# Optimization experiments

Hardware: AMD Instinct MI355X
Metric: run time of the kernel (lower is better)

The kernel has to match this reference:

```python
import jax, jax.numpy as jnp
import numpy as np

SQRT_HALF = np.float32(np.sqrt(0.5))
H_AX, W_AX = 2, 3


def _refl_idx(idx, r):
    # symmetric extension with edge repetition (np.pad mode='symmetric'),
    # identical to dtcwt's reflect(idx, -0.5, r-0.5). Static numpy computation.
    idx = np.mod(idx, 2 * r)
    return np.where(idx < r, idx, 2 * r - 1 - idx)


def _filt(X, h, axis):
    # Non-decimating 1-D filtering (dtcwt colfilter/rowfilter): symmetric pad by
    # len(h)//2, true convolution, 'valid' -> output same length as input.
    X = jnp.moveaxis(X, axis, -1)
    m = h.shape[0]
    m2 = m // 2
    L = X.shape[-1]
    Xp = jnp.pad(X, [(0, 0)] * (X.ndim - 1) + [(m2, m2)], mode='symmetric')
    out = sum(h[m - 1 - j] * Xp[..., j:j + L] for j in range(m))  # flip -> convolution
    return jnp.moveaxis(out, -1, axis)


def _dfilt(X, ha, hb, highpass, axis):
    # Decimate-by-2 dual-tree filtering (dtcwt coldfilt/rowdfilt).
    # ha filters one polyphase stream, hb the other; outputs are interleaved.
    X = jnp.moveaxis(X, axis, -1)
    r = X.shape[-1]
    assert r % 4 == 0, 'filtered dim must be a multiple of 4'
    m = ha.shape[0]
    m2 = m // 2
    xe = _refl_idx(np.arange(-m, r + m), r)        # symmetric-extended indices
    t = np.arange(5, r + 2 * m - 2, 4)             # 0-based MATLAB t = 6:4:r+2m-2
    hao, hae = ha[0::2], ha[1::2]
    hbo, hbe = hb[0::2], hb[1::2]

    def cv(rows, f):
        # 'valid' true convolution along gathered (stride-4) sample sequence
        A = X[..., rows]
        Lout = rows.shape[0] - m2 + 1              # == r // 4
        return sum(f[m2 - 1 - j] * A[..., j:j + Lout] for j in range(m2))

    ya = cv(xe[t - 1], hao) + cv(xe[t - 3], hae)
    yb = cv(xe[t], hbo) + cv(xe[t - 2], hbe)
    first, second = (yb, ya) if highpass else (ya, yb)
    Y = jnp.stack([first, second], axis=-1).reshape(X.shape[:-1] + (r // 2,))
    return jnp.moveaxis(Y, -1, axis)


def _q2c(y):
    # quads -> two complex subimages: p = (a+jb)/sqrt2, q = (d-jc)/sqrt2; z = p -/+ q
    a = y[..., 0::2, 0::2]
    b = y[..., 0::2, 1::2]
    c = y[..., 1::2, 0::2]
    d = y[..., 1::2, 1::2]
    z1 = ((a - d) * SQRT_HALF, (b + c) * SQRT_HALF)
    z2 = ((a + d) * SQRT_HALF, (b - c) * SQRT_HALF)
    return z1, z2


def _bands_to_yh(lh, hl, hh):
    # orientation order 15,45,75,105,135,165 degrees; output [N,C,6,H',W',2]
    (r15, i15), (r165, i165) = _q2c(lh)
    (r45, i45), (r135, i135) = _q2c(hh)
    (r75, i75), (r105, i105) = _q2c(hl)
    reals = jnp.stack([r15, r45, r75, r105, r135, r165], axis=2)
    imags = jnp.stack([i15, i45, i75, i105, i135, i165], axis=2)
    return jnp.stack([reals, imags], axis=-1)


def _dtcwt_fwd(x, h0o, h1o, h0a, h0b, h1a, h1b, J=3):
    # Level 1: non-decimating biorthogonal filters
    lo = _filt(x, h0o, W_AX)
    hi = _filt(x, h1o, W_AX)
    ll = _filt(lo, h0o, H_AX)
    yh = [_bands_to_yh(_filt(lo, h1o, H_AX),   # lh
                       _filt(hi, h0o, H_AX),   # hl
                       _filt(hi, h1o, H_AX))]  # hh
    # Levels 2..J: decimating qshift filters
    for _ in range(1, J):
        lo = _dfilt(ll, h0b, h0a, False, W_AX)
        hi = _dfilt(ll, h1b, h1a, True, W_AX)
        ll = _dfilt(lo, h0b, h0a, False, H_AX)
        yh.append(_bands_to_yh(_dfilt(lo, h1b, h1a, True, H_AX),
                               _dfilt(hi, h0b, h0a, False, H_AX),
                               _dfilt(hi, h1b, h1a, True, H_AX)))
    return (ll, *yh)


def setup_inputs() -> dict:
    key = jax.random.key(0)
    ks = jax.random.split(key, 5)
    x = jax.random.normal(ks[0], (4, 16, 512, 512), dtype=jnp.float32)

    def mk(k, n):
        h = jax.random.normal(k, (n,), dtype=jnp.float32)
        return h / jnp.linalg.norm(h)  # unit-norm to keep levels well scaled

    h0o = mk(ks[1], 5)
    h1o = mk(ks[2], 7)
    h0a = mk(ks[3], 10)
    h1a = mk(ks[4], 10)
    h0b = h0a[::-1]  # dual-tree property: tree-b = time-reversed tree-a
    h1b = h1a[::-1]
    return {'x': x, 'h0o': h0o, 'h1o': h1o, 'h0a': h0a, 'h0b': h0b,
            'h1a': h1a, 'h1b': h1b}


def reference(x, h0o, h1o, h0a, h0b, h1a, h1b):
    # Returns (yl, yh_level1, yh_level2, yh_level3)
    return _dtcwt_fwd(x, h0o, h1o, h0a, h0b, h1a, h1b, J=3)
```

## Files before the change

### kernel.cpp

```cpp
#include <hip/hip_runtime.h>

#define S1 512
#define NIMG 64

__device__ __forceinline__ int refl(int a, int L) {
    a = (a < 0) ? (-a - 1) : a;
    a = (a >= L) ? (2 * L - 1 - a) : a;
    return a;
}

__global__ __launch_bounds__(256) void k_level1(
    const float* __restrict__ x,
    const float* __restrict__ h0o_g, const float* __restrict__ h1o_g,
    float* __restrict__ ll1, float* __restrict__ yh0)
{
    __shared__ float xs[70 * 71];
    __shared__ float lo_s[70 * 65];
    __shared__ float hi_s[70 * 65];

    const int t  = threadIdx.x;
    const int c0 = blockIdx.x * 64;
    const int r0 = blockIdx.y * 64;
    const int n  = blockIdx.z;
    const float* __restrict__ xn = x + (size_t)n * (S1 * S1);

    float f0[5], f1[7];
#pragma unroll
    for (int i = 0; i < 5; ++i) f0[i] = h0o_g[i];
#pragma unroll
    for (int i = 0; i < 7; ++i) f1[i] = h1o_g[i];

    for (int l = t; l < 70 * 70; l += 256) {
        int rl = l / 70, cl = l - rl * 70;
        int ar = refl(r0 - 3 + rl, S1);
        int ac = refl(c0 - 3 + cl, S1);
        xs[rl * 71 + cl] = xn[(size_t)ar * S1 + ac];
    }
    __syncthreads();

    for (int l = t; l < 70 * 64; l += 256) {
        int rl = l >> 6, cl = l & 63;
        const float* xr = &xs[rl * 71 + cl];
        float v0 = xr[0], v1 = xr[1], v2 = xr[2], v3 = xr[3],
              v4 = xr[4], v5 = xr[5], v6 = xr[6];
        float lo = f0[0]*v5 + f0[1]*v4 + f0[2]*v3 + f0[3]*v2 + f0[4]*v1;
        float hi = f1[0]*v6 + f1[1]*v5 + f1[2]*v4 + f1[3]*v3 + f1[4]*v2
                 + f1[5]*v1 + f1[6]*v0;
        lo_s[rl * 65 + cl] = lo;
        hi_s[rl * 65 + cl] = hi;
    }
    __syncthreads();

    const float SQH = 0.70710678118654752440f;
    float* __restrict__ yhn = yh0 + (size_t)n * (6 * 256 * 256 * 2);
    float* __restrict__ lln = ll1 + (size_t)n * (S1 * S1);
    for (int q = t; q < 32 * 32; q += 256) {
        int qi = q >> 5, qj = q & 31;
        float llq[2][2], lhq[2][2], hlq[2][2], hhq[2][2];
#pragma unroll
        for (int cc = 0; cc < 2; ++cc) {
            const int col = 2 * qj + cc;
            float L[8];
#pragma unroll
            for (int j = 0; j < 8; ++j) L[j] = lo_s[(2 * qi + j) * 65 + col];
            llq[0][cc] = f0[0]*L[5] + f0[1]*L[4] + f0[2]*L[3] + f0[3]*L[2] + f0[4]*L[1];
            llq[1][cc] = f0[0]*L[6] + f0[1]*L[5] + f0[2]*L[4] + f0[3]*L[3] + f0[4]*L[2];
            lhq[0][cc] = f1[0]*L[6] + f1[1]*L[5] + f1[2]*L[4] + f1[3]*L[3]
                       + f1[4]*L[2] + f1[5]*L[1] + f1[6]*L[0];
            lhq[1][cc] = f1[0]*L[7] + f1[1]*L[6] + f1[2]*L[5] + f1[3]*L[4]
                       + f1[4]*L[3] + f1[5]*L[2] + f1[6]*L[1];
#pragma unroll
            for (int j = 0; j < 8; ++j) L[j] = hi_s[(2 * qi + j) * 65 + col];
            hlq[0][cc] = f0[0]*L[5] + f0[1]*L[4] + f0[2]*L[3] + f0[3]*L[2] + f0[4]*L[1];
            hlq[1][cc] = f0[0]*L[6] + f0[1]*L[5] + f0[2]*L[4] + f0[3]*L[3] + f0[4]*L[2];
            hhq[0][cc] = f1[0]*L[6] + f1[1]*L[5] + f1[2]*L[4] + f1[3]*L[3]
                       + f1[4]*L[2] + f1[5]*L[1] + f1[6]*L[0];
            hhq[1][cc] = f1[0]*L[7] + f1[1]*L[6] + f1[2]*L[5] + f1[3]*L[4]
                       + f1[4]*L[3] + f1[5]*L[2] + f1[6]*L[1];
        }
        const int oy = r0 + 2 * qi, ox = c0 + 2 * qj;
        float2 w;
        w.x = llq[0][0]; w.y = llq[0][1];
        *(float2*)&lln[(size_t)oy * S1 + ox] = w;
        w.x = llq[1][0]; w.y = llq[1][1];
        *(float2*)&lln[(size_t)(oy + 1) * S1 + ox] = w;

        const int i2 = (r0 >> 1) + qi, j2 = (c0 >> 1) + qj;
        const size_t bs = 256 * 256 * 2;
        float* __restrict__ p = yhn + ((size_t)i2 * 256 + j2) * 2;
        w.x = (lhq[0][0] - lhq[1][1]) * SQH; w.y = (lhq[0][1] + lhq[1][0]) * SQH; *(float2*)(p + 0 * bs) = w;
        w.x = (hhq[0][0] - hhq[1][1]) * SQH; w.y = (hhq[0][1] + hhq[1][0]) * SQH; *(float2*)(p + 1 * bs) = w;
        w.x = (hlq[0][0] - hlq[1][1]) * SQH; w.y = (hlq[0][1] + hlq[1][0]) * SQH; *(float2*)(p + 2 * bs) = w;
        w.x = (hlq[0][0] + hlq[1][1]) * SQH; w.y = (hlq[0][1] - hlq[1][0]) * SQH; *(float2*)(p + 3 * bs) = w;
        w.x = (hhq[0][0] + hhq[1][1]) * SQH; w.y = (hhq[0][1] - hhq[1][0]) * SQH; *(float2*)(p + 4 * bs) = w;
        w.x = (lhq[0][0] + lhq[1][1]) * SQH; w.y = (lhq[0][1] - lhq[1][0]) * SQH; *(float2*)(p + 5 * bs) = w;
    }
}

__global__ __launch_bounds__(256) void k_dfilt(
    const float* __restrict__ X, const int r,
    const float* __restrict__ h0a_g, const float* __restrict__ h0b_g,
    const float* __restrict__ h1a_g, const float* __restrict__ h1b_g,
    float* __restrict__ llo, float* __restrict__ yh)
{
    __shared__ float Xs[80 * 84];
    __shared__ float lo_s[80 * 33];
    __shared__ float hi_s[80 * 33];

    const int t  = threadIdx.x;
    const int x0 = blockIdx.x * 32;
    const int y0 = blockIdx.y * 32;
    const int n  = blockIdx.z;
    const float* __restrict__ Xn = X + (size_t)n * r * r;
    const int cb = 2 * x0 - 8, rb = 2 * y0 - 8;

    float fa0[10], fb0[10], fa1[10], fb1[10];
#pragma unroll
    for (int i = 0; i < 10; ++i) {
        fa0[i] = h0a_g[i]; fb0[i] = h0b_g[i];
        fa1[i] = h1a_g[i]; fb1[i] = h1b_g[i];
    }

    for (int l = t; l < 80 * 80; l += 256) {
        int rl = l / 80, cl = l - rl * 80;
        int ar = refl(rb + rl, r);
        int ac = refl(cb + cl, r);
        Xs[rl * 84 + cl] = Xn[(size_t)ar * r + ac];
    }
    __syncthreads();

    {
        const int cl = t & 31;
        const bool ev = (cl & 1) == 0;
        float cL[20], cH[20];
#pragma unroll
        for (int j = 0; j < 20; ++j) { cL[j] = 0.f; cH[j] = 0.f; }
#pragma unroll
        for (int k = 0; k < 10; ++k) {
            cL[18 - 2 * k] = ev ? fb0[k] : 0.f;
            cL[19 - 2 * k] = ev ? cL[19 - 2 * k] : fa0[k];
            cH[19 - 2 * k] = ev ? fa1[k] : cH[19 - 2 * k];
            cH[18 - 2 * k] = ev ? cH[18 - 2 * k] : fb1[k];
        }
        const int base = 2 * cl - (ev ? 0 : 2);
        for (int rl = (t >> 5); rl < 80; rl += 8) {
            const float* Vp = &Xs[rl * 84 + base];
            float V[20];
#pragma unroll
            for (int j = 0; j < 5; ++j) {
                float4 v = *(const float4*)(Vp + 4 * j);
                V[4*j+0] = v.x; V[4*j+1] = v.y; V[4*j+2] = v.z; V[4*j+3] = v.w;
            }
            float lo = 0.f, hi = 0.f;
#pragma unroll
            for (int j = 0; j < 20; ++j) { lo += cL[j] * V[j]; hi += cH[j] * V[j]; }
            lo_s[rl * 33 + cl] = lo;
            hi_s[rl * 33 + cl] = hi;
        }
    }
    __syncthreads();

    {
        const int qi = t >> 4, qj = t & 15;
        float llq[2][2], lhq[2][2], hlq[2][2], hhq[2][2];
#pragma unroll
        for (int cc = 0; cc < 2; ++cc) {
            const int col = 2 * qj + cc;
            float L[20];
#pragma unroll
            for (int j = 0; j < 20; ++j) L[j] = lo_s[(4 * qi + j) * 33 + col];
            float ll_e = 0.f, ll_o = 0.f, lh_e = 0.f, lh_o = 0.f;
#pragma unroll
            for (int k = 0; k < 10; ++k) {
                float le = L[18 - 2 * k], lod = L[19 - 2 * k];
                ll_e += fb0[k] * le;
                ll_o += fa0[k] * lod;
                lh_e += fa1[k] * lod;
                lh_o += fb1[k] * le;
            }
            llq[0][cc] = ll_e; llq[1][cc] = ll_o;
            lhq[0][cc] = lh_e; lhq[1][cc] = lh_o;
#pragma unroll
            for (int j = 0; j < 20; ++j) L[j] = hi_s[(4 * qi + j) * 33 + col];
            float hl_e = 0.f, hl_o = 0.f, hh_e = 0.f, hh_o = 0.f;
#pragma unroll
            for (int k = 0; k < 10; ++k) {
                float he = L[18 - 2 * k], ho = L[19 - 2 * k];
                hl_e += fb0[k] * he;
                hl_o += fa0[k] * ho;
                hh_e += fa1[k] * ho;
                hh_o += fb1[k] * he;
            }
            hlq[0][cc] = hl_e; hlq[1][cc] = hl_o;
            hhq[0][cc] = hh_e; hhq[1][cc] = hh_o;
        }

        const int R = r >> 1, R2 = r >> 2;
        const int oy = y0 + 2 * qi, ox = x0 + 2 * qj;
        float2 w;
        w.x = llq[0][0]; w.y = llq[0][1];
        *(float2*)&llo[((size_t)n * R + oy) * R + ox] = w;
        w.x = llq[1][0]; w.y = llq[1][1];
        *(float2*)&llo[((size_t)n * R + oy + 1) * R + ox] = w;

        const float SQH = 0.70710678118654752440f;
        const int i2 = (y0 >> 1) + qi, j2 = (x0 >> 1) + qj;
        const size_t bs = (size_t)R2 * R2 * 2;
        float* __restrict__ p = yh + (size_t)n * 6 * bs + ((size_t)i2 * R2 + j2) * 2;
        w.x = (lhq[0][0] - lhq[1][1]) * SQH; w.y = (lhq[0][1] + lhq[1][0]) * SQH; *(float2*)(p + 0 * bs) = w;
        w.x = (hhq[0][0] - hhq[1][1]) * SQH; w.y = (hhq[0][1] + hhq[1][0]) * SQH; *(float2*)(p + 1 * bs) = w;
        w.x = (hlq[0][0] - hlq[1][1]) * SQH; w.y = (hlq[0][1] + hlq[1][0]) * SQH; *(float2*)(p + 2 * bs) = w;
        w.x = (hlq[0][0] + hlq[1][1]) * SQH; w.y = (hlq[0][1] - hlq[1][0]) * SQH; *(float2*)(p + 3 * bs) = w;
        w.x = (hhq[0][0] + hhq[1][1]) * SQH; w.y = (hhq[0][1] - hhq[1][0]) * SQH; *(float2*)(p + 4 * bs) = w;
        w.x = (lhq[0][0] + lhq[1][1]) * SQH; w.y = (lhq[0][1] - lhq[1][0]) * SQH; *(float2*)(p + 5 * bs) = w;
    }
}

extern "C" void kernel_launch(void* const* d_in, const int* in_sizes, int n_in,
                              void* d_out, int out_size, void* d_ws, size_t ws_size,
                              hipStream_t stream) {
    const float* x   = (const float*)d_in[0];
    const float* h0o = (const float*)d_in[1];
    const float* h1o = (const float*)d_in[2];
    const float* h0a = (const float*)d_in[3];
    const float* h0b = (const float*)d_in[4];
    const float* h1a = (const float*)d_in[5];
    const float* h1b = (const float*)d_in[6];

    float* out = (float*)d_out;
    float* ll3 = out;
    float* yh0 = out + 1048576;
    float* yh1 = out + 51380224;
    float* yh2 = out + 63963136;

    float* ll1 = (float*)d_ws;
    float* ll2 = ll1 + 16777216;

    k_level1<<<dim3(8, 8, NIMG), 256, 0, stream>>>(x, h0o, h1o, ll1, yh0);
    k_dfilt<<<dim3(8, 8, NIMG), 256, 0, stream>>>(ll1, 512, h0a, h0b, h1a, h1b, ll2, yh1);
    k_dfilt<<<dim3(4, 4, NIMG), 256, 0, stream>>>(ll2, 256, h0a, h0b, h1a, h1b, ll3, yh2);
}
```

Baseline: 428.6 us.

## Vectorize tile loads and LDS accesses, split level-1 tile into row halves

The level-1 kernel now processes its 64x64 tile in two 32-row halves, which shrinks shared memory per block. Interior tiles load input columns with float4 global reads, and the row-filter and quad stages use float4 LDS reads and writes. The decimating kernel also uses a float4 fast path for interior loads, and each thread computes an even/odd output pair from one 20-sample window, stored and re-read as float2 from a padded layout. The aim is fewer memory instructions and better occupancy. The cost is recomputing halo rows in each level-1 half and an extra sync per half.

```diff
diff --git a/kernel.cpp b/kernel.cpp
--- a/kernel.cpp
+++ b/kernel.cpp
@@ -14,15 +14,17 @@
     const float* __restrict__ h0o_g, const float* __restrict__ h1o_g,
     float* __restrict__ ll1, float* __restrict__ yh0)
 {
-    __shared__ float xs[70 * 71];
-    __shared__ float lo_s[70 * 65];
-    __shared__ float hi_s[70 * 65];
+    __shared__ float xs[38 * 72];
+    __shared__ float lo_s[38 * 68];
+    __shared__ float hi_s[38 * 68];
 
     const int t  = threadIdx.x;
     const int c0 = blockIdx.x * 64;
     const int r0 = blockIdx.y * 64;
     const int n  = blockIdx.z;
-    const float* __restrict__ xn = x + (size_t)n * (S1 * S1);
+    const float* __restrict__ xn  = x   + (size_t)n * (S1 * S1);
+    float* __restrict__ lln       = ll1 + (size_t)n * (S1 * S1);
+    float* __restrict__ yhn       = yh0 + (size_t)n * (6 * 256 * 256 * 2);
 
     float f0[5], f1[7];
 #pragma unroll
@@ -30,70 +32,115 @@
 #pragma unroll
     for (int i = 0; i < 7; ++i) f1[i] = h1o_g[i];
 
-    for (int l = t; l < 70 * 70; l += 256) {
-        int rl = l / 70, cl = l - rl * 70;
-        int ar = refl(r0 - 3 + rl, S1);
-        int ac = refl(c0 - 3 + cl, S1);
-        xs[rl * 71 + cl] = xn[(size_t)ar * S1 + ac];
-    }
-    __syncthreads();
-
-    for (int l = t; l < 70 * 64; l += 256) {
-        int rl = l >> 6, cl = l & 63;
-        const float* xr = &xs[rl * 71 + cl];
-        float v0 = xr[0], v1 = xr[1], v2 = xr[2], v3 = xr[3],
-              v4 = xr[4], v5 = xr[5], v6 = xr[6];
-        float lo = f0[0]*v5 + f0[1]*v4 + f0[2]*v3 + f0[3]*v2 + f0[4]*v1;
-        float hi = f1[0]*v6 + f1[1]*v5 + f1[2]*v4 + f1[3]*v3 + f1[4]*v2
-                 + f1[5]*v1 + f1[6]*v0;
-        lo_s[rl * 65 + cl] = lo;
-        hi_s[rl * 65 + cl] = hi;
-    }
-    __syncthreads();
-
+    const bool colfast = (c0 >= 4) && (c0 + 67 < S1);
     const float SQH = 0.70710678118654752440f;
-    float* __restrict__ yhn = yh0 + (size_t)n * (6 * 256 * 256 * 2);
-    float* __restrict__ lln = ll1 + (size_t)n * (S1 * S1);
-    for (int q = t; q < 32 * 32; q += 256) {
-        int qi = q >> 5, qj = q & 31;
-        float llq[2][2], lhq[2][2], hlq[2][2], hhq[2][2];
-#pragma unroll
-        for (int cc = 0; cc < 2; ++cc) {
-            const int col = 2 * qj + cc;
-            float L[8];
-#pragma unroll
-            for (int j = 0; j < 8; ++j) L[j] = lo_s[(2 * qi + j) * 65 + col];
-            llq[0][cc] = f0[0]*L[5] + f0[1]*L[4] + f0[2]*L[3] + f0[3]*L[2] + f0[4]*L[1];
-            llq[1][cc] = f0[0]*L[6] + f0[1]*L[5] + f0[2]*L[4] + f0[3]*L[3] + f0[4]*L[2];
-            lhq[0][cc] = f1[0]*L[6] + f1[1]*L[5] + f1[2]*L[4] + f1[3]*L[3]
-                       + f1[4]*L[2] + f1[5]*L[1] + f1[6]*L[0];
-            lhq[1][cc] = f1[0]*L[7] + f1[1]*L[6] + f1[2]*L[5] + f1[3]*L[4]
-                       + f1[4]*L[3] + f1[5]*L[2] + f1[6]*L[1];
-#pragma unroll
-            for (int j = 0; j < 8; ++j) L[j] = hi_s[(2 * qi + j) * 65 + col];
-            hlq[0][cc] = f0[0]*L[5] + f0[1]*L[4] + f0[2]*L[3] + f0[3]*L[2] + f0[4]*L[1];
-            hlq[1][cc] = f0[0]*L[6] + f0[1]*L[5] + f0[2]*L[4] + f0[3]*L[3] + f0[4]*L[2];
-            hhq[0][cc] = f1[0]*L[6] + f1[1]*L[5] + f1[2]*L[4] + f1[3]*L[3]
-                       + f1[4]*L[2] + f1[5]*L[1] + f1[6]*L[0];
-            hhq[1][cc] = f1[0]*L[7] + f1[1]*L[6] + f1[2]*L[5] + f1[3]*L[4]
-                       + f1[4]*L[3] + f1[5]*L[2] + f1[6]*L[1];
-        }
-        const int oy = r0 + 2 * qi, ox = c0 + 2 * qj;
-        float2 w;
-        w.x = llq[0][0]; w.y = llq[0][1];
-        *(float2*)&lln[(size_t)oy * S1 + ox] = w;
-        w.x = llq[1][0]; w.y = llq[1][1];
-        *(float2*)&lln[(size_t)(oy + 1) * S1 + ox] = w;
-
-        const int i2 = (r0 >> 1) + qi, j2 = (c0 >> 1) + qj;
-        const size_t bs = 256 * 256 * 2;
-        float* __restrict__ p = yhn + ((size_t)i2 * 256 + j2) * 2;
-        w.x = (lhq[0][0] - lhq[1][1]) * SQH; w.y = (lhq[0][1] + lhq[1][0]) * SQH; *(float2*)(p + 0 * bs) = w;
-        w.x = (hhq[0][0] - hhq[1][1]) * SQH; w.y = (hhq[0][1] + hhq[1][0]) * SQH; *(float2*)(p + 1 * bs) = w;
-        w.x = (hlq[0][0] - hlq[1][1]) * SQH; w.y = (hlq[0][1] + hlq[1][0]) * SQH; *(float2*)(p + 2 * bs) = w;
-        w.x = (hlq[0][0] + hlq[1][1]) * SQH; w.y = (hlq[0][1] - hlq[1][0]) * SQH; *(float2*)(p + 3 * bs) = w;
-        w.x = (hhq[0][0] + hhq[1][1]) * SQH; w.y = (hhq[0][1] - hhq[1][0]) * SQH; *(float2*)(p + 4 * bs) = w;
-        w.x = (lhq[0][0] + lhq[1][1]) * SQH; w.y = (lhq[0][1] - lhq[1][0]) * SQH; *(float2*)(p + 5 * bs) = w;
+
+    for (int h = 0; h < 2; ++h) {
+        const int gr0 = r0 + 32 * h - 3;
+
+        if (colfast) {
+            for (int l = t; l < 38 * 18; l += 256) {
+                int rl = l / 18, cf = l - rl * 18;
+                int ar = refl(gr0 + rl, S1);
+                float4 v = *(const float4*)&xn[(size_t)ar * S1 + (c0 - 4) + 4 * cf];
+                *(float4*)&xs[rl * 72 + 4 * cf] = v;
+            }
+        } else {
+            for (int l = t; l < 38 * 72; l += 256) {
+                int rl = l / 72, cl = l - rl * 72;
+                xs[rl * 72 + cl] =
+                    xn[(size_t)refl(gr0 + rl, S1) * S1 + refl(c0 - 4 + cl, S1)];
+            }
+        }
+        __syncthreads();
+
+        for (int l = t; l < 38 * 16; l += 256) {
+            int rl = l >> 4, cg = l & 15;
+            const float* p = &xs[rl * 72 + 4 * cg];
+            float4 va = *(const float4*)p;
+            float4 vb = *(const float4*)(p + 4);
+            float4 vc = *(const float4*)(p + 8);
+            float V[12] = {va.x, va.y, va.z, va.w, vb.x, vb.y, vb.z, vb.w,
+                           vc.x, vc.y, vc.z, vc.w};
+            float lov[4], hiv[4];
+#pragma unroll
+            for (int cc = 0; cc < 4; ++cc) {
+                lov[cc] = f0[0]*V[cc+6] + f0[1]*V[cc+5] + f0[2]*V[cc+4]
+                        + f0[3]*V[cc+3] + f0[4]*V[cc+2];
+                hiv[cc] = f1[0]*V[cc+7] + f1[1]*V[cc+6] + f1[2]*V[cc+5]
+                        + f1[3]*V[cc+4] + f1[4]*V[cc+3] + f1[5]*V[cc+2]
+                        + f1[6]*V[cc+1];
+            }
+            *(float4*)&lo_s[rl * 68 + 4 * cg] = make_float4(lov[0], lov[1], lov[2], lov[3]);
+            *(float4*)&hi_s[rl * 68 + 4 * cg] = make_float4(hiv[0], hiv[1], hiv[2], hiv[3]);
+        }
+        __syncthreads();
+
+        {
+            const int qi = t >> 4, cg = t & 15;
+            float4 Lv[8];
+            float llv[2][4], lhv[2][4], hlv[2][4], hhv[2][4];
+
+#pragma unroll
+            for (int j = 0; j < 8; ++j)
+                Lv[j] = *(const float4*)&lo_s[(2 * qi + j) * 68 + 4 * cg];
+            {
+                const float* L = (const float*)Lv;
+#pragma unroll
+                for (int cc = 0; cc < 4; ++cc) {
+                    float Lc[8];
+#pragma unroll
+                    for (int j = 0; j < 8; ++j) Lc[j] = L[4 * j + cc];
+                    llv[0][cc] = f0[0]*Lc[5] + f0[1]*Lc[4] + f0[2]*Lc[3] + f0[3]*Lc[2] + f0[4]*Lc[1];
+                    llv[1][cc] = f0[0]*Lc[6] + f0[1]*Lc[5] + f0[2]*Lc[4] + f0[3]*Lc[3] + f0[4]*Lc[2];
+                    lhv[0][cc] = f1[0]*Lc[6] + f1[1]*Lc[5] + f1[2]*Lc[4] + f1[3]*Lc[3]
+                               + f1[4]*Lc[2] + f1[5]*Lc[1] + f1[6]*Lc[0];
+                    lhv[1][cc] = f1[0]*Lc[7] + f1[1]*Lc[6] + f1[2]*Lc[5] + f1[3]*Lc[4]
+                               + f1[4]*Lc[3] + f1[5]*Lc[2] + f1[6]*Lc[1];
+                }
+            }
+#pragma unroll
+            for (int j = 0; j < 8; ++j)
+                Lv[j] = *(const float4*)&hi_s[(2 * qi + j) * 68 + 4 * cg];
+            {
+                const float* L = (const float*)Lv;
+#pragma unroll
+                for (int cc = 0; cc < 4; ++cc) {
+                    float Lc[8];
+#pragma unroll
+                    for (int j = 0; j < 8; ++j) Lc[j] = L[4 * j + cc];
+                    hlv[0][cc] = f0[0]*Lc[5] + f0[1]*Lc[4] + f0[2]*Lc[3] + f0[3]*Lc[2] + f0[4]*Lc[1];
+                    hlv[1][cc] = f0[0]*Lc[6] + f0[1]*Lc[5] + f0[2]*Lc[4] + f0[3]*Lc[3] + f0[4]*Lc[2];
+                    hhv[0][cc] = f1[0]*Lc[6] + f1[1]*Lc[5] + f1[2]*Lc[4] + f1[3]*Lc[3]
+                               + f1[4]*Lc[2] + f1[5]*Lc[1] + f1[6]*Lc[0];
+                    hhv[1][cc] = f1[0]*Lc[7] + f1[1]*Lc[6] + f1[2]*Lc[5] + f1[3]*Lc[4]
+                               + f1[4]*Lc[3] + f1[5]*Lc[2] + f1[6]*Lc[1];
+                }
+            }
+
+            const int oy = r0 + 32 * h + 2 * qi, ox = c0 + 4 * cg;
+            *(float4*)&lln[(size_t)oy * S1 + ox] =
+                make_float4(llv[0][0], llv[0][1], llv[0][2], llv[0][3]);
+            *(float4*)&lln[(size_t)(oy + 1) * S1 + ox] =
+                make_float4(llv[1][0], llv[1][1], llv[1][2], llv[1][3]);
+
+            const int i2 = (r0 >> 1) + 16 * h + qi, j2 = (c0 >> 1) + 2 * cg;
+            const size_t bs = 256 * 256 * 2;
+            float* __restrict__ p = yhn + ((size_t)i2 * 256 + j2) * 2;
+#define BAND_Z1(X0, X1) make_float4((X0[0]-X1[1])*SQH, (X0[1]+X1[0])*SQH, \
+                                    (X0[2]-X1[3])*SQH, (X0[3]+X1[2])*SQH)
+#define BAND_Z2(X0, X1) make_float4((X0[0]+X1[1])*SQH, (X0[1]-X1[0])*SQH, \
+                                    (X0[2]+X1[3])*SQH, (X0[3]-X1[2])*SQH)
+            *(float4*)(p + 0 * bs) = BAND_Z1(lhv[0], lhv[1]);
+            *(float4*)(p + 1 * bs) = BAND_Z1(hhv[0], hhv[1]);
+            *(float4*)(p + 2 * bs) = BAND_Z1(hlv[0], hlv[1]);
+            *(float4*)(p + 3 * bs) = BAND_Z2(hlv[0], hlv[1]);
+            *(float4*)(p + 4 * bs) = BAND_Z2(hhv[0], hhv[1]);
+            *(float4*)(p + 5 * bs) = BAND_Z2(lhv[0], lhv[1]);
+#undef BAND_Z1
+#undef BAND_Z2
+        }
+        __syncthreads();
     }
 }
 
@@ -104,8 +151,8 @@
     float* __restrict__ llo, float* __restrict__ yh)
 {
     __shared__ float Xs[80 * 84];
-    __shared__ float lo_s[80 * 33];
-    __shared__ float hi_s[80 * 33];
+    __shared__ float lo_s[80 * 36];
+    __shared__ float hi_s[80 * 36];
 
     const int t  = threadIdx.x;
     const int x0 = blockIdx.x * 32;
@@ -121,92 +168,102 @@
         fa1[i] = h1a_g[i]; fb1[i] = h1b_g[i];
     }
 
-    for (int l = t; l < 80 * 80; l += 256) {
-        int rl = l / 80, cl = l - rl * 80;
-        int ar = refl(rb + rl, r);
-        int ac = refl(cb + cl, r);
-        Xs[rl * 84 + cl] = Xn[(size_t)ar * r + ac];
+    const bool colfast = (cb >= 0) && (cb + 79 < r);
+
+    if (colfast) {
+        for (int l = t; l < 80 * 20; l += 256) {
+            int rl = l / 20, cf = l - rl * 20;
+            int ar = refl(rb + rl, r);
+            float4 v = *(const float4*)&Xn[(size_t)ar * r + cb + 4 * cf];
+            *(float4*)&Xs[rl * 84 + 4 * cf] = v;
+        }
+    } else {
+        for (int l = t; l < 80 * 80; l += 256) {
+            int rl = l / 80, cl = l - rl * 80;
+            Xs[rl * 84 + cl] = Xn[(size_t)refl(rb + rl, r) * r + refl(cb + cl, r)];
+        }
     }
     __syncthreads();
 
+    for (int l = t; l < 80 * 16; l += 256) {
+        int rl = l >> 4, cp = l & 15;
+        const float* p = &Xs[rl * 84 + 4 * cp];
+        float V[20];
+#pragma unroll
+        for (int j = 0; j < 5; ++j) {
+            float4 v = *(const float4*)(p + 4 * j);
+            V[4*j+0] = v.x; V[4*j+1] = v.y; V[4*j+2] = v.z; V[4*j+3] = v.w;
+        }
+        float lo_e = 0.f, lo_o = 0.f, hi_e = 0.f, hi_o = 0.f;
+#pragma unroll
+        for (int k = 0; k < 10; ++k) {
+            float ve = V[18 - 2 * k], vo = V[19 - 2 * k];
+            lo_e += fb0[k] * ve;
+            lo_o += fa0[k] * vo;
+            hi_e += fa1[k] * vo;
+            hi_o += fb1[k] * ve;
+        }
+        *(float2*)&lo_s[rl * 36 + 2 * cp] = make_float2(lo_e, lo_o);
+        *(float2*)&hi_s[rl * 36 + 2 * cp] = make_float2(hi_e, hi_o);
+    }
+    __syncthreads();
+
     {
-        const int cl = t & 31;
-        const bool ev = (cl & 1) == 0;
-        float cL[20], cH[20];
-#pragma unroll
-        for (int j = 0; j < 20; ++j) { cL[j] = 0.f; cH[j] = 0.f; }
-#pragma unroll
-        for (int k = 0; k < 10; ++k) {
-            cL[18 - 2 * k] = ev ? fb0[k] : 0.f;
-            cL[19 - 2 * k] = ev ? cL[19 - 2 * k] : fa0[k];
-            cH[19 - 2 * k] = ev ? fa1[k] : cH[19 - 2 * k];
-            cH[18 - 2 * k] = ev ? cH[18 - 2 * k] : fb1[k];
-        }
-        const int base = 2 * cl - (ev ? 0 : 2);
-        for (int rl = (t >> 5); rl < 80; rl += 8) {
-            const float* Vp = &Xs[rl * 84 + base];
-            float V[20];
-#pragma unroll
-            for (int j = 0; j < 5; ++j) {
-                float4 v = *(const float4*)(Vp + 4 * j);
-                V[4*j+0] = v.x; V[4*j+1] = v.y; V[4*j+2] = v.z; V[4*j+3] = v.w;
-            }
-            float lo = 0.f, hi = 0.f;
-#pragma unroll
-            for (int j = 0; j < 20; ++j) { lo += cL[j] * V[j]; hi += cH[j] * V[j]; }
-            lo_s[rl * 33 + cl] = lo;
-            hi_s[rl * 33 + cl] = hi;
-        }
-    }
-    __syncthreads();
-
-    {
-        const int qi = t >> 4, qj = t & 15;
+        const int qi = t >> 4, cg = t & 15;
+        float2 Lv[20];
         float llq[2][2], lhq[2][2], hlq[2][2], hhq[2][2];
-#pragma unroll
-        for (int cc = 0; cc < 2; ++cc) {
-            const int col = 2 * qj + cc;
-            float L[20];
-#pragma unroll
-            for (int j = 0; j < 20; ++j) L[j] = lo_s[(4 * qi + j) * 33 + col];
-            float ll_e = 0.f, ll_o = 0.f, lh_e = 0.f, lh_o = 0.f;
-#pragma unroll
-            for (int k = 0; k < 10; ++k) {
-                float le = L[18 - 2 * k], lod = L[19 - 2 * k];
-                ll_e += fb0[k] * le;
-                ll_o += fa0[k] * lod;
-                lh_e += fa1[k] * lod;
-                lh_o += fb1[k] * le;
-            }
-            llq[0][cc] = ll_e; llq[1][cc] = ll_o;
-            lhq[0][cc] = lh_e; lhq[1][cc] = lh_o;
-#pragma unroll
-            for (int j = 0; j < 20; ++j) L[j] = hi_s[(4 * qi + j) * 33 + col];
-            float hl_e = 0.f, hl_o = 0.f, hh_e = 0.f, hh_o = 0.f;
-#pragma unroll
-            for (int k = 0; k < 10; ++k) {
-                float he = L[18 - 2 * k], ho = L[19 - 2 * k];
-                hl_e += fb0[k] * he;
-                hl_o += fa0[k] * ho;
-                hh_e += fa1[k] * ho;
-                hh_o += fb1[k] * he;
-            }
-            hlq[0][cc] = hl_e; hlq[1][cc] = hl_o;
-            hhq[0][cc] = hh_e; hhq[1][cc] = hh_o;
+
+#pragma unroll
+        for (int j = 0; j < 20; ++j)
+            Lv[j] = *(const float2*)&lo_s[(4 * qi + j) * 36 + 2 * cg];
+        {
+            const float* L = (const float*)Lv;
+#pragma unroll
+            for (int cc = 0; cc < 2; ++cc) {
+                float e0 = 0.f, o0 = 0.f, e1 = 0.f, o1 = 0.f;
+#pragma unroll
+                for (int k = 0; k < 10; ++k) {
+                    float le = L[(18 - 2 * k) * 2 + cc], lo = L[(19 - 2 * k) * 2 + cc];
+                    e0 += fb0[k] * le;
+                    o0 += fa0[k] * lo;
+                    e1 += fa1[k] * lo;
+                    o1 += fb1[k] * le;
+                }
+                llq[0][cc] = e0; llq[1][cc] = o0;
+                lhq[0][cc] = e1; lhq[1][cc] = o1;
+            }
+        }
+#pragma unroll
+        for (int j = 0; j < 20; ++j)
+            Lv[j] = *(const float2*)&hi_s[(4 * qi + j) * 36 + 2 * cg];
+        {
+            const float* L = (const float*)Lv;
+#pragma unroll
+            for (int cc = 0; cc < 2; ++cc) {
+                float e0 = 0.f, o0 = 0.f, e1 = 0.f, o1 = 0.f;
+#pragma unroll
+                for (int k = 0; k < 10; ++k) {
+                    float he = L[(18 - 2 * k) * 2 + cc], ho = L[(19 - 2 * k) * 2 + cc];
+                    e0 += fb0[k] * he;
+                    o0 += fa0[k] * ho;
+                    e1 += fa1[k] * ho;
+                    o1 += fb1[k] * he;
+                }
+                hlq[0][cc] = e0; hlq[1][cc] = o0;
+                hhq[0][cc] = e1; hhq[1][cc] = o1;
+            }
         }
 
         const int R = r >> 1, R2 = r >> 2;
-        const int oy = y0 + 2 * qi, ox = x0 + 2 * qj;
-        float2 w;
-        w.x = llq[0][0]; w.y = llq[0][1];
-        *(float2*)&llo[((size_t)n * R + oy) * R + ox] = w;
-        w.x = llq[1][0]; w.y = llq[1][1];
-        *(float2*)&llo[((size_t)n * R + oy + 1) * R + ox] = w;
+        const int oy = y0 + 2 * qi, ox = x0 + 2 * cg;
+        *(float2*)&llo[((size_t)n * R + oy) * R + ox]     = make_float2(llq[0][0], llq[0][1]);
+        *(float2*)&llo[((size_t)n * R + oy + 1) * R + ox] = make_float2(llq[1][0], llq[1][1]);
 
         const float SQH = 0.70710678118654752440f;
-        const int i2 = (y0 >> 1) + qi, j2 = (x0 >> 1) + qj;
+        const int i2 = (y0 >> 1) + qi, j2 = (x0 >> 1) + cg;
         const size_t bs = (size_t)R2 * R2 * 2;
         float* __restrict__ p = yh + (size_t)n * 6 * bs + ((size_t)i2 * R2 + j2) * 2;
+        float2 w;
         w.x = (lhq[0][0] - lhq[1][1]) * SQH; w.y = (lhq[0][1] + lhq[1][0]) * SQH; *(float2*)(p + 0 * bs) = w;
         w.x = (hhq[0][0] - hhq[1][1]) * SQH; w.y = (hhq[0][1] + hhq[1][0]) * SQH; *(float2*)(p + 1 * bs) = w;
         w.x = (hlq[0][0] - hlq[1][1]) * SQH; w.y = (hlq[0][1] + hlq[1][0]) * SQH; *(float2*)(p + 2 * bs) = w;
```

Result: no change. 421.6 us (-1.6%).
